# Performance work log

Hardware: AMD Instinct MI355X
Metric: run time of the kernel (lower is better)

The kernel has to match this reference:

```python
import jax, jax.numpy as jnp
import numpy as np

# 9 jitter shifts: (L, R, T, B) padding applied to `input`; `target` gets the
# opposite padding (L<->R, T<->B swapped), producing a 1-pixel relative shift.
SHIFTS = ((0, 0, 0, 0), (0, 0, 1, 0), (0, 0, 0, 1), (1, 0, 0, 0), (0, 1, 0, 0),
          (1, 0, 1, 0), (0, 1, 0, 1), (0, 1, 1, 0), (1, 0, 0, 1))
SMIN_K = 32.0


def _shifted_diff(inp, tgt, L, R, T, B):
    # get_opposite in the original simply swaps the pad pair
    Lt, Rt = R, L
    Tt, Bt = B, T
    # ConstantPad2d((L,R,T,B)) pads last dim by (L,R), second-to-last by (T,B)
    pi = jnp.pad(inp, ((0, 0), (T, B), (L, R)))
    pt = jnp.pad(tgt, ((0, 0), (Tt, Bt), (Lt, Rt)))  # same padded shape
    d = jnp.abs(pi - pt)
    n, m, k = d.shape
    # crop back to the original (batch, max_len, dim) window
    return d[:, T:m - B, L:k - R]


def setup_inputs() -> dict:
    key = jax.random.key(0)
    k1, k2 = jax.random.split(key)
    B, T, D = 64, 2048, 80
    return {
        "input": jax.random.normal(k1, (B, T, D), dtype=jnp.float32),
        "target": jax.random.normal(k2, (B, T, D), dtype=jnp.float32),
    }


def reference(input, target):
    # (batch, max_len, dim, 9): abs-diff for each of the 9 relative shifts
    diffs = jnp.stack(
        [_shifted_diff(input, target, L, R, T, B) for (L, R, T, B) in SHIFTS],
        axis=-1,
    )
    # smooth minimum over the 9 shifts: -log(sum(exp(-k*t)))/k (stable via logsumexp)
    sm = -jax.scipy.special.logsumexp(-SMIN_K * diffs, axis=-1) / SMIN_K
    center = diffs[..., 0]  # unshifted abs-diff
    # average of the center diff and the smooth-min, reduced to a scalar loss
    return 0.5 * (jnp.mean(center) + jnp.mean(sm))
```

## Files before the change

### kernel.cpp

```cpp
#include <hip/hip_runtime.h>
#include <math.h>

#define BATCH 64
#define TLEN 2048
#define DIM 80
#define DQ (DIM / 4)
#define TT 8
#define TCHUNKS (TLEN / TT)
#define THREADS 256
#define NSTRIPS (BATCH * TCHUNKS * DQ)
#define NBLOCKS (NSTRIPS / THREADS)

#define SMIN_C  46.166241308446828f
#define SMIN_RC 0.02166084939249829f

__device__ __forceinline__ void load_row(float r[6], const float* __restrict__ base,
                                         int t, int q) {
    if (t >= 0 && t < TLEN) {
        const float* p = base + (size_t)t * DIM;
        const float4 v = *(const float4*)p;
        r[0] = (q > 0)      ? p[-1] : 0.f;
        r[1] = v.x; r[2] = v.y; r[3] = v.z; r[4] = v.w;
        r[5] = (q < DQ - 1) ? p[4]  : 0.f;
    } else {
#pragma unroll
        for (int i = 0; i < 6; ++i) r[i] = 0.f;
    }
}

__device__ __forceinline__ float elem_loss(float x, const float* rm, const float* r0,
                                           const float* rp, int e) {
    float v[9];
#pragma unroll
    for (int i = 0; i < 3; ++i) {
        v[0 + i] = fabsf(x - rm[e + i]);
        v[3 + i] = fabsf(x - r0[e + i]);
        v[6 + i] = fabsf(x - rp[e + i]);
    }
    const float center = v[4];
    float m = fminf(fminf(fminf(v[0], v[1]), fminf(v[2], v[3])),
                    fminf(fminf(v[4], v[5]), fminf(v[6], v[7])));
    m = fminf(m, v[8]);
    float S = 0.f;
#pragma unroll
    for (int s = 0; s < 9; ++s)
        S += __builtin_amdgcn_exp2f(SMIN_C * (m - v[s]));
    const float sm = m - __builtin_amdgcn_logf(S) * SMIN_RC;
    return center + sm;
}

__global__ __launch_bounds__(THREADS) void jitter_kernel(
    const float* __restrict__ inp, const float* __restrict__ tgt,
    float* __restrict__ ws)
{
    __shared__ float wsum[THREADS / 64];

    const int n   = blockIdx.x * THREADS + threadIdx.x;
    const int q   = n % DQ;
    const int rem = n / DQ;
    const int tc  = rem % TCHUNKS;
    const int b   = rem / TCHUNKS;
    const int t0  = tc * TT;
    const int d0  = q * 4;

    const float* tgb = tgt + (size_t)b * TLEN * DIM + d0;
    const float* inb = inp + (size_t)b * TLEN * DIM + d0;

    float rm[6], r0[6], rp[6];
    load_row(rm, tgb, t0 - 1, q);
    load_row(r0, tgb, t0,     q);

    float acc = 0.f;
#pragma unroll
    for (int lt = 0; lt < TT; ++lt) {
        load_row(rp, tgb, t0 + lt + 1, q);
        const float4 in4 = *(const float4*)(inb + (size_t)(t0 + lt) * DIM);
        acc += elem_loss(in4.x, rm, r0, rp, 0);
        acc += elem_loss(in4.y, rm, r0, rp, 1);
        acc += elem_loss(in4.z, rm, r0, rp, 2);
        acc += elem_loss(in4.w, rm, r0, rp, 3);
#pragma unroll
        for (int i = 0; i < 6; ++i) { rm[i] = r0[i]; r0[i] = rp[i]; }
    }

#pragma unroll
    for (int off = 32; off > 0; off >>= 1)
        acc += __shfl_down(acc, off, 64);
    const int lane = threadIdx.x & 63, wid = threadIdx.x >> 6;
    if (lane == 0) wsum[wid] = acc;
    __syncthreads();
    if (threadIdx.x == 0) {
        float tot = 0.f;
#pragma unroll
        for (int w = 0; w < THREADS / 64; ++w) tot += wsum[w];
        ws[blockIdx.x] = tot;
    }
}

__global__ __launch_bounds__(256) void reduce_kernel(const float* __restrict__ ws,
                                                     float* __restrict__ out) {
    __shared__ float wsum[4];
    float s = 0.f;
    for (int i = threadIdx.x; i < NBLOCKS; i += 256) s += ws[i];
#pragma unroll
    for (int off = 32; off > 0; off >>= 1)
        s += __shfl_down(s, off, 64);
    const int lane = threadIdx.x & 63, wid = threadIdx.x >> 6;
    if (lane == 0) wsum[wid] = s;
    __syncthreads();
    if (threadIdx.x == 0) {
        float tot = wsum[0] + wsum[1] + wsum[2] + wsum[3];
        out[0] = tot * (0.5f / (float)((size_t)BATCH * TLEN * DIM));
    }
}

extern "C" void kernel_launch(void* const* d_in, const int* in_sizes, int n_in,
                              void* d_out, int out_size, void* d_ws, size_t ws_size,
                              hipStream_t stream) {
    const float* inp = (const float*)d_in[0];
    const float* tgt = (const float*)d_in[1];
    float* ws  = (float*)d_ws;
    float* out = (float*)d_out;

    jitter_kernel<<<NBLOCKS, THREADS, 0, stream>>>(inp, tgt, ws);
    reduce_kernel<<<1, 256, 0, stream>>>(ws, out);
}
```

Measured before the change: 112.1 us.

## Widen per-thread strip to 8 columns and fuse final reduction via atomics

New measurement: 128.3 us. +14.4%, slower.

```diff
diff --git a/kernel.cpp b/kernel.cpp
--- a/kernel.cpp
+++ b/kernel.cpp
@@ -4,27 +4,29 @@
 #define BATCH 64
 #define TLEN 2048
 #define DIM 80
-#define DQ (DIM / 4)
+#define DO8 (DIM / 8)
 #define TT 8
 #define TCHUNKS (TLEN / TT)
 #define THREADS 256
-#define NSTRIPS (BATCH * TCHUNKS * DQ)
+#define NSTRIPS (BATCH * TCHUNKS * DO8)
 #define NBLOCKS (NSTRIPS / THREADS)
 
 #define SMIN_C  46.166241308446828f
 #define SMIN_RC 0.02166084939249829f
 
-__device__ __forceinline__ void load_row(float r[6], const float* __restrict__ base,
-                                         int t, int q) {
+__device__ __forceinline__ void load_row8(float r[10], const float* __restrict__ base,
+                                          int t, int q8) {
     if (t >= 0 && t < TLEN) {
         const float* p = base + (size_t)t * DIM;
-        const float4 v = *(const float4*)p;
-        r[0] = (q > 0)      ? p[-1] : 0.f;
-        r[1] = v.x; r[2] = v.y; r[3] = v.z; r[4] = v.w;
-        r[5] = (q < DQ - 1) ? p[4]  : 0.f;
+        const float4 a = *(const float4*)p;
+        const float4 c = *(const float4*)(p + 4);
+        r[0] = (q8 > 0)       ? p[-1] : 0.f;
+        r[1] = a.x; r[2] = a.y; r[3] = a.z; r[4] = a.w;
+        r[5] = c.x; r[6] = c.y; r[7] = c.z; r[8] = c.w;
+        r[9] = (q8 < DO8 - 1) ? p[8]  : 0.f;
     } else {
 #pragma unroll
-        for (int i = 0; i < 6; ++i) r[i] = 0.f;
+        for (int i = 0; i < 10; ++i) r[i] = 0.f;
     }
 }
 
@@ -41,46 +43,53 @@
     float m = fminf(fminf(fminf(v[0], v[1]), fminf(v[2], v[3])),
                     fminf(fminf(v[4], v[5]), fminf(v[6], v[7])));
     m = fminf(m, v[8]);
+    const float cm = SMIN_C * m;
     float S = 0.f;
 #pragma unroll
     for (int s = 0; s < 9; ++s)
-        S += __builtin_amdgcn_exp2f(SMIN_C * (m - v[s]));
+        S += __builtin_amdgcn_exp2f(fmaf(-SMIN_C, v[s], cm));
     const float sm = m - __builtin_amdgcn_logf(S) * SMIN_RC;
     return center + sm;
 }
 
 __global__ __launch_bounds__(THREADS) void jitter_kernel(
     const float* __restrict__ inp, const float* __restrict__ tgt,
-    float* __restrict__ ws)
+    float* __restrict__ ws, float* __restrict__ out)
 {
     __shared__ float wsum[THREADS / 64];
 
     const int n   = blockIdx.x * THREADS + threadIdx.x;
-    const int q   = n % DQ;
-    const int rem = n / DQ;
+    const int q8  = n % DO8;
+    const int rem = n / DO8;
     const int tc  = rem % TCHUNKS;
     const int b   = rem / TCHUNKS;
     const int t0  = tc * TT;
-    const int d0  = q * 4;
+    const int d0  = q8 * 8;
 
     const float* tgb = tgt + (size_t)b * TLEN * DIM + d0;
     const float* inb = inp + (size_t)b * TLEN * DIM + d0;
 
-    float rm[6], r0[6], rp[6];
-    load_row(rm, tgb, t0 - 1, q);
-    load_row(r0, tgb, t0,     q);
+    float rm[10], r0[10], rp[10];
+    load_row8(rm, tgb, t0 - 1, q8);
+    load_row8(r0, tgb, t0,     q8);
 
     float acc = 0.f;
 #pragma unroll
     for (int lt = 0; lt < TT; ++lt) {
-        load_row(rp, tgb, t0 + lt + 1, q);
-        const float4 in4 = *(const float4*)(inb + (size_t)(t0 + lt) * DIM);
-        acc += elem_loss(in4.x, rm, r0, rp, 0);
-        acc += elem_loss(in4.y, rm, r0, rp, 1);
-        acc += elem_loss(in4.z, rm, r0, rp, 2);
-        acc += elem_loss(in4.w, rm, r0, rp, 3);
+        load_row8(rp, tgb, t0 + lt + 1, q8);
+        const float* ip = inb + (size_t)(t0 + lt) * DIM;
+        const float4 ia = *(const float4*)ip;
+        const float4 ic = *(const float4*)(ip + 4);
+        acc += elem_loss(ia.x, rm, r0, rp, 0);
+        acc += elem_loss(ia.y, rm, r0, rp, 1);
+        acc += elem_loss(ia.z, rm, r0, rp, 2);
+        acc += elem_loss(ia.w, rm, r0, rp, 3);
+        acc += elem_loss(ic.x, rm, r0, rp, 4);
+        acc += elem_loss(ic.y, rm, r0, rp, 5);
+        acc += elem_loss(ic.z, rm, r0, rp, 6);
+        acc += elem_loss(ic.w, rm, r0, rp, 7);
 #pragma unroll
-        for (int i = 0; i < 6; ++i) { rm[i] = r0[i]; r0[i] = rp[i]; }
+        for (int i = 0; i < 10; ++i) { rm[i] = r0[i]; r0[i] = rp[i]; }
     }
 
 #pragma unroll
@@ -93,25 +102,19 @@
         float tot = 0.f;
 #pragma unroll
         for (int w = 0; w < THREADS / 64; ++w) tot += wsum[w];
-        ws[blockIdx.x] = tot;
+        atomicAdd(&ws[0], tot);
+        __threadfence();
+        int old = atomicAdd((int*)ws + 1, 1);
+        if (old == NBLOCKS - 1) {
+            __threadfence();
+            const float s = atomicAdd(&ws[0], 0.f);
+            out[0] = s * (0.5f / (float)((size_t)BATCH * TLEN * DIM));
+        }
     }
 }
 
-__global__ __launch_bounds__(256) void reduce_kernel(const float* __restrict__ ws,
-                                                     float* __restrict__ out) {
-    __shared__ float wsum[4];
-    float s = 0.f;
-    for (int i = threadIdx.x; i < NBLOCKS; i += 256) s += ws[i];
-#pragma unroll
-    for (int off = 32; off > 0; off >>= 1)
-        s += __shfl_down(s, off, 64);
-    const int lane = threadIdx.x & 63, wid = threadIdx.x >> 6;
-    if (lane == 0) wsum[wid] = s;
-    __syncthreads();
-    if (threadIdx.x == 0) {
-        float tot = wsum[0] + wsum[1] + wsum[2] + wsum[3];
-        out[0] = tot * (0.5f / (float)((size_t)BATCH * TLEN * DIM));
-    }
+__global__ void zero_kernel(float* ws) {
+    if (threadIdx.x < 2) ws[threadIdx.x] = 0.f;
 }
 
 extern "C" void kernel_launch(void* const* d_in, const int* in_sizes, int n_in,
@@ -122,6 +125,6 @@
     float* ws  = (float*)d_ws;
     float* out = (float*)d_out;
 
-    jitter_kernel<<<NBLOCKS, THREADS, 0, stream>>>(inp, tgt, ws);
-    reduce_kernel<<<1, 256, 0, stream>>>(ws, out);
+    zero_kernel<<<1, 64, 0, stream>>>(ws);
+    jitter_kernel<<<NBLOCKS, THREADS, 0, stream>>>(inp, tgt, ws, out);
 }
```
